# Kernel tuning notes

Hardware: AMD Instinct MI355X
Metric: run time of the kernel (lower is better)

## Reference

```python
import jax, jax.numpy as jnp
import numpy as np

VOCAB = 50257
D = 1024
EDGES = [0, 20000, 40000, VOCAB]  # cluster boundaries
HSZ = [1024, 256, 64]             # D // 4**i per cluster


def setup_inputs() -> dict:
    key = jax.random.key(0)
    ks = jax.random.split(key, 8)
    emb_input = jax.random.randint(ks[0], (8, 2048), 0, VOCAB, dtype=jnp.int64)
    inp = {"emb_input": emb_input}
    for i in range(3):
        vsz = EDGES[i + 1] - EDGES[i]
        h = HSZ[i]
        inp[f"emb{i}"] = jax.random.normal(ks[1 + 2 * i], (vsz, h), dtype=jnp.float32) * 0.02
        # nn.Linear(h, D, bias=False) weight has shape [D, h]
        inp[f"w{i}"] = jax.random.normal(ks[2 + 2 * i], (D, h), dtype=jnp.float32) * 0.02
    return inp


def reference(emb_input, emb0, w0, emb1, w1, emb2, w2):
    B, S = emb_input.shape
    idx = emb_input.reshape(-1)  # [N]
    clusters = [(emb0, w0), (emb1, w1), (emb2, w2)]
    out = jnp.zeros((idx.shape[0], D), dtype=jnp.float32)
    for i, (emb, w) in enumerate(clusters):
        lo, hi = EDGES[i], EDGES[i + 1]
        mask = (idx >= lo) & (idx < hi)                       # [N]
        local = jnp.clip(idx - lo, 0, emb.shape[0] - 1)       # in-range gather ids
        h = emb[local]                                        # [N, hsz_i]
        proj = jnp.einsum('nh,dh->nd', h, w)                  # [N, D]
        out = out + jnp.where(mask[:, None], proj, 0.0)
    return out.reshape(B, S, D)
```

## Files before the change

### kernel.cpp

```cpp
#include <hip/hip_runtime.h>
#include <stdint.h>

#define DOUT 1024
#define NMAX 16384

typedef __attribute__((ext_vector_type(8))) short short8;
typedef __attribute__((ext_vector_type(4))) float floatx4;

__device__ __forceinline__ unsigned short f2bf(float f) {
  union { float f; uint32_t u; } v;
  v.f = f;
  return (unsigned short)((v.u + 0x7FFFu + ((v.u >> 16) & 1u)) >> 16);
}

__global__ __launch_bounds__(256) void classify_cvt_kernel(
    const int* __restrict__ idx, int* __restrict__ cnt,
    int* __restrict__ bucket, int* __restrict__ blocal, int N,
    const float* __restrict__ w0, const float* __restrict__ w1,
    const float* __restrict__ w2, unsigned short* __restrict__ wb0,
    unsigned short* __restrict__ wb1, unsigned short* __restrict__ wb2) {
  if (blockIdx.x < 64) {
    int n = blockIdx.x * 256 + threadIdx.x;
    int lane = threadIdx.x & 63;
    int c = -1, v = 0;
    if (n < N) {
      v = idx[n];
      c = (v < 20000) ? 0 : ((v < 40000) ? 1 : 2);
    }
#pragma unroll
    for (int k = 0; k < 3; ++k) {
      unsigned long long m = __ballot(c == k);
      if (c == k) {
        int leader = __ffsll((unsigned long long)m) - 1;
        int base = 0;
        if (lane == leader) base = atomicAdd(&cnt[k], (int)__popcll(m));
        base = __shfl(base, leader);
        int rank = (int)__popcll(m & ((1ull << (unsigned)lane) - 1ull));
        int lo = (k == 0) ? 0 : (k == 1) ? 20000 : 40000;
        bucket[k * NMAX + base + rank] = n;
        blocal[k * NMAX + base + rank] = v - lo;
      }
    }
  } else {
    int i = (blockIdx.x - 64) * 256 + threadIdx.x;
    if (i >= 344064) return;
    const float4* src;
    ushort4* dst;
    if (i < 262144) {
      src = (const float4*)w0 + i;
      dst = (ushort4*)wb0 + i;
    } else if (i < 327680) {
      src = (const float4*)w1 + (i - 262144);
      dst = (ushort4*)wb1 + (i - 262144);
    } else {
      src = (const float4*)w2 + (i - 327680);
      dst = (ushort4*)wb2 + (i - 327680);
    }
    float4 v = *src;
    ushort4 o;
    o.x = f2bf(v.x); o.y = f2bf(v.y); o.z = f2bf(v.z); o.w = f2bf(v.w);
    *dst = o;
  }
}

__global__ __launch_bounds__(256) void gather_fused(
    const float* __restrict__ emb0, const float* __restrict__ emb1,
    const float* __restrict__ emb2, const int* __restrict__ blocal,
    const int* __restrict__ cnt, unsigned short* __restrict__ a0,
    unsigned short* __restrict__ a1, unsigned short* __restrict__ a2) {
  const int z = blockIdx.z;
  const int hshift = 10 - 2 * z;
  const float* emb = (z == 0) ? emb0 : (z == 1) ? emb1 : emb2;
  unsigned short* acomp = (z == 0) ? a0 : (z == 1) ? a1 : a2;
  const int* bl = blocal + z * NMAX;
  const int count = cnt[z];
  const int h4s = hshift - 2;
  const int total = count << h4s;
  for (int i = blockIdx.x * 256 + threadIdx.x; i < total; i += gridDim.x * 256) {
    int row = i >> h4s;
    int k4 = i & ((1 << h4s) - 1);
    int loc = bl[row];
    float4 v = ((const float4*)(emb + ((size_t)loc << hshift)))[k4];
    ushort4 o;
    o.x = f2bf(v.x); o.y = f2bf(v.y); o.z = f2bf(v.z); o.w = f2bf(v.w);
    ((ushort4*)(acomp + ((size_t)row << hshift)))[k4] = o;
  }
}

template <int H>
__device__ __forceinline__ void gemm_body(
    const unsigned short* __restrict__ A, const unsigned short* __restrict__ B,
    int count, const int* __restrict__ bucket, float* __restrict__ out,
    unsigned short* As, unsigned short* Bs, int* rowTok) {
  const int m0 = blockIdx.y * 64;
  if (m0 >= count) return;
  const int n0 = blockIdx.x * 128;

  const int tid = threadIdx.x;
  const int wave = tid >> 6;
  const int lane = tid & 63;
  const int quad = lane >> 4;
  const int l16 = lane & 15;
  const int wm = wave & 1;
  const int wn = wave >> 1;

  if (tid < 64) {
    int m = m0 + tid;
    rowTok[tid] = (m < count) ? bucket[m] : -1;
  }

  floatx4 acc[2][4];
#pragma unroll
  for (int i = 0; i < 2; ++i)
#pragma unroll
    for (int j = 0; j < 4; ++j) acc[i][j] = (floatx4){0.f, 0.f, 0.f, 0.f};

  const char* Ab = (const char*)A;
  const char* Bb = (const char*)B;
  const int row_lo = tid >> 2;
  const int ck = tid & 3;

  for (int k0 = 0; k0 < H; k0 += 64) {
    __syncthreads();
#pragma unroll
    for (int t = 0; t < 2; ++t) {
      const void* ga = Ab + ((size_t)(m0 + row_lo) * H + k0 + t * 32) * 2 + ck * 16;
      void* la = (char*)As + (t * 4096 + wave * 1024);
      __builtin_amdgcn_global_load_lds(
          (const __attribute__((address_space(1))) void*)ga,
          (__attribute__((address_space(3))) void*)la, 16, 0, 0);
    }
#pragma unroll
    for (int t = 0; t < 2; ++t)
#pragma unroll
      for (int p = 0; p < 2; ++p) {
        const void* gb =
            Bb + ((size_t)(n0 + p * 64 + row_lo) * H + k0 + t * 32) * 2 + ck * 16;
        void* lb = (char*)Bs + (t * 8192 + p * 4096 + wave * 1024);
        __builtin_amdgcn_global_load_lds(
            (const __attribute__((address_space(1))) void*)gb,
            (__attribute__((address_space(3))) void*)lb, 16, 0, 0);
      }
    __syncthreads();

#pragma unroll
    for (int t = 0; t < 2; ++t) {
      short8 af[2], bf[4];
#pragma unroll
      for (int mi = 0; mi < 2; ++mi)
        af[mi] = *(const short8*)&As[t * 2048 + (wm * 32 + mi * 16 + l16) * 32 + quad * 8];
#pragma unroll
      for (int ni = 0; ni < 4; ++ni)
        bf[ni] = *(const short8*)&Bs[t * 4096 + (wn * 64 + ni * 16 + l16) * 32 + quad * 8];
#pragma unroll
      for (int mi = 0; mi < 2; ++mi)
#pragma unroll
        for (int ni = 0; ni < 4; ++ni)
          acc[mi][ni] = __builtin_amdgcn_mfma_f32_16x16x32_bf16(
              af[mi], bf[ni], acc[mi][ni], 0, 0, 0);
    }
  }

  const int colBase = n0 + wn * 64 + l16;
#pragma unroll
  for (int mi = 0; mi < 2; ++mi) {
#pragma unroll
    for (int r = 0; r < 4; ++r) {
      int tok = rowTok[wm * 32 + mi * 16 + quad * 4 + r];
      if (tok >= 0) {
        float* o = out + (size_t)tok * DOUT + colBase;
#pragma unroll
        for (int ni = 0; ni < 4; ++ni) o[ni * 16] = acc[mi][ni][r];
      }
    }
  }
}

__global__ __launch_bounds__(256) void gemm_fused(
    const unsigned short* __restrict__ a0, const unsigned short* __restrict__ a1,
    const unsigned short* __restrict__ a2, const unsigned short* __restrict__ wb0,
    const unsigned short* __restrict__ wb1, const unsigned short* __restrict__ wb2,
    const int* __restrict__ cnt, const int* __restrict__ bucket,
    float* __restrict__ out) {
  __shared__ __align__(16) unsigned short As[2 * 64 * 32];
  __shared__ __align__(16) unsigned short Bs[2 * 128 * 32];
  __shared__ int rowTok[64];

  const int z = blockIdx.z;
  if (z == 0)
    gemm_body<1024>(a0, wb0, cnt[0], bucket + 0 * NMAX, out, As, Bs, rowTok);
  else if (z == 1)
    gemm_body<256>(a1, wb1, cnt[1], bucket + 1 * NMAX, out, As, Bs, rowTok);
  else
    gemm_body<64>(a2, wb2, cnt[2], bucket + 2 * NMAX, out, As, Bs, rowTok);
}

extern "C" void kernel_launch(void* const* d_in, const int* in_sizes, int n_in,
                              void* d_out, int out_size, void* d_ws, size_t ws_size,
                              hipStream_t stream) {
  const int* idx = (const int*)d_in[0];
  const float* emb0 = (const float*)d_in[1];
  const float* w0 = (const float*)d_in[2];
  const float* emb1 = (const float*)d_in[3];
  const float* w1 = (const float*)d_in[4];
  const float* emb2 = (const float*)d_in[5];
  const float* w2 = (const float*)d_in[6];
  float* out = (float*)d_out;
  const int N = in_sizes[0];

  char* ws = (char*)d_ws;
  int* cnt = (int*)ws;
  int* bucket = (int*)(ws + 1024);
  int* blocal = bucket + 3 * NMAX;
  size_t off = 1024 + (size_t)6 * NMAX * 4;
  off = (off + 255) & ~(size_t)255;
  unsigned short* wb0 = (unsigned short*)(ws + off); off += (size_t)DOUT * 1024 * 2;
  unsigned short* wb1 = (unsigned short*)(ws + off); off += (size_t)DOUT * 256 * 2;
  unsigned short* wb2 = (unsigned short*)(ws + off); off += (size_t)DOUT * 64 * 2;
  off = (off + 255) & ~(size_t)255;
  unsigned short* a0 = (unsigned short*)(ws + off); off += (size_t)NMAX * 1024 * 2;
  unsigned short* a1 = (unsigned short*)(ws + off); off += (size_t)NMAX * 256 * 2;
  unsigned short* a2 = (unsigned short*)(ws + off); off += (size_t)NMAX * 64 * 2;

  hipMemsetAsync(cnt, 0, 16 * sizeof(int), stream);

  classify_cvt_kernel<<<64 + 1344, 256, 0, stream>>>(
      idx, cnt, bucket, blocal, N, w0, w1, w2, wb0, wb1, wb2);

  dim3 ggrid(512, 1, 3);
  gather_fused<<<ggrid, 256, 0, stream>>>(emb0, emb1, emb2, blocal, cnt, a0, a1, a2);

  dim3 grid(DOUT / 128, NMAX / 64, 3);
  gemm_fused<<<grid, 256, 0, stream>>>(a0, a1, a2, wb0, wb1, wb2, cnt, bucket, out);
}
```

Before: 208.2 us.

## Fuse embedding gather and bf16 conversion into the GEMM A-tile load

```diff
diff --git a/kernel.cpp b/kernel.cpp
--- a/kernel.cpp
+++ b/kernel.cpp
@@ -1,4 +1,5 @@
 #include <hip/hip_runtime.h>
+#include <hip/hip_bf16.h>
 #include <stdint.h>
 
 #define DOUT 1024
@@ -11,6 +12,16 @@
   union { float f; uint32_t u; } v;
   v.f = f;
   return (unsigned short)((v.u + 0x7FFFu + ((v.u >> 16) & 1u)) >> 16);
+}
+
+__device__ __forceinline__ short8 cvt8(float4 a, float4 b) {
+  __hip_bfloat162 p0 = __float22bfloat162_rn(make_float2(a.x, a.y));
+  __hip_bfloat162 p1 = __float22bfloat162_rn(make_float2(a.z, a.w));
+  __hip_bfloat162 p2 = __float22bfloat162_rn(make_float2(b.x, b.y));
+  __hip_bfloat162 p3 = __float22bfloat162_rn(make_float2(b.z, b.w));
+  union { __hip_bfloat162 h[4]; short8 s; } u;
+  u.h[0] = p0; u.h[1] = p1; u.h[2] = p2; u.h[3] = p3;
+  return u.s;
 }
 
 __global__ __launch_bounds__(256) void classify_cvt_kernel(
@@ -63,35 +74,12 @@
   }
 }
 
-__global__ __launch_bounds__(256) void gather_fused(
-    const float* __restrict__ emb0, const float* __restrict__ emb1,
-    const float* __restrict__ emb2, const int* __restrict__ blocal,
-    const int* __restrict__ cnt, unsigned short* __restrict__ a0,
-    unsigned short* __restrict__ a1, unsigned short* __restrict__ a2) {
-  const int z = blockIdx.z;
-  const int hshift = 10 - 2 * z;
-  const float* emb = (z == 0) ? emb0 : (z == 1) ? emb1 : emb2;
-  unsigned short* acomp = (z == 0) ? a0 : (z == 1) ? a1 : a2;
-  const int* bl = blocal + z * NMAX;
-  const int count = cnt[z];
-  const int h4s = hshift - 2;
-  const int total = count << h4s;
-  for (int i = blockIdx.x * 256 + threadIdx.x; i < total; i += gridDim.x * 256) {
-    int row = i >> h4s;
-    int k4 = i & ((1 << h4s) - 1);
-    int loc = bl[row];
-    float4 v = ((const float4*)(emb + ((size_t)loc << hshift)))[k4];
-    ushort4 o;
-    o.x = f2bf(v.x); o.y = f2bf(v.y); o.z = f2bf(v.z); o.w = f2bf(v.w);
-    ((ushort4*)(acomp + ((size_t)row << hshift)))[k4] = o;
-  }
-}
-
 template <int H>
 __device__ __forceinline__ void gemm_body(
-    const unsigned short* __restrict__ A, const unsigned short* __restrict__ B,
-    int count, const int* __restrict__ bucket, float* __restrict__ out,
-    unsigned short* As, unsigned short* Bs, int* rowTok) {
+    const float* __restrict__ emb, const unsigned short* __restrict__ B,
+    int count, const int* __restrict__ bucket, const int* __restrict__ blocal,
+    float* __restrict__ out, unsigned short* As, unsigned short* Bs,
+    int* rowTok, int* rowLoc) {
   const int m0 = blockIdx.y * 64;
   if (m0 >= count) return;
   const int n0 = blockIdx.x * 128;
@@ -107,7 +95,9 @@
   if (tid < 64) {
     int m = m0 + tid;
     rowTok[tid] = (m < count) ? bucket[m] : -1;
-  }
+    rowLoc[tid] = (m < count) ? blocal[m] : 0;
+  }
+  __syncthreads();
 
   floatx4 acc[2][4];
 #pragma unroll
@@ -115,20 +105,20 @@
 #pragma unroll
     for (int j = 0; j < 4; ++j) acc[i][j] = (floatx4){0.f, 0.f, 0.f, 0.f};
 
-  const char* Ab = (const char*)A;
   const char* Bb = (const char*)B;
   const int row_lo = tid >> 2;
   const int ck = tid & 3;
 
+  const float* arow = emb + (size_t)rowLoc[row_lo] * H + ck * 8;
+
   for (int k0 = 0; k0 < H; k0 += 64) {
     __syncthreads();
 #pragma unroll
     for (int t = 0; t < 2; ++t) {
-      const void* ga = Ab + ((size_t)(m0 + row_lo) * H + k0 + t * 32) * 2 + ck * 16;
-      void* la = (char*)As + (t * 4096 + wave * 1024);
-      __builtin_amdgcn_global_load_lds(
-          (const __attribute__((address_space(1))) void*)ga,
-          (__attribute__((address_space(3))) void*)la, 16, 0, 0);
+      const float* src = arow + k0 + t * 32;
+      float4 v0 = *(const float4*)src;
+      float4 v1 = *(const float4*)(src + 4);
+      *(short8*)&As[t * 2048 + row_lo * 32 + ck * 8] = cvt8(v0, v1);
     }
 #pragma unroll
     for (int t = 0; t < 2; ++t)
@@ -177,22 +167,26 @@
 }
 
 __global__ __launch_bounds__(256) void gemm_fused(
-    const unsigned short* __restrict__ a0, const unsigned short* __restrict__ a1,
-    const unsigned short* __restrict__ a2, const unsigned short* __restrict__ wb0,
+    const float* __restrict__ emb0, const float* __restrict__ emb1,
+    const float* __restrict__ emb2, const unsigned short* __restrict__ wb0,
     const unsigned short* __restrict__ wb1, const unsigned short* __restrict__ wb2,
     const int* __restrict__ cnt, const int* __restrict__ bucket,
-    float* __restrict__ out) {
+    const int* __restrict__ blocal, float* __restrict__ out) {
   __shared__ __align__(16) unsigned short As[2 * 64 * 32];
   __shared__ __align__(16) unsigned short Bs[2 * 128 * 32];
   __shared__ int rowTok[64];
+  __shared__ int rowLoc[64];
 
   const int z = blockIdx.z;
   if (z == 0)
-    gemm_body<1024>(a0, wb0, cnt[0], bucket + 0 * NMAX, out, As, Bs, rowTok);
+    gemm_body<1024>(emb0, wb0, cnt[0], bucket + 0 * NMAX, blocal + 0 * NMAX,
+                    out, As, Bs, rowTok, rowLoc);
   else if (z == 1)
-    gemm_body<256>(a1, wb1, cnt[1], bucket + 1 * NMAX, out, As, Bs, rowTok);
+    gemm_body<256>(emb1, wb1, cnt[1], bucket + 1 * NMAX, blocal + 1 * NMAX,
+                   out, As, Bs, rowTok, rowLoc);
   else
-    gemm_body<64>(a2, wb2, cnt[2], bucket + 2 * NMAX, out, As, Bs, rowTok);
+    gemm_body<64>(emb2, wb2, cnt[2], bucket + 2 * NMAX, blocal + 2 * NMAX,
+                  out, As, Bs, rowTok, rowLoc);
 }
 
 extern "C" void kernel_launch(void* const* d_in, const int* in_sizes, int n_in,
@@ -217,19 +211,13 @@
   unsigned short* wb0 = (unsigned short*)(ws + off); off += (size_t)DOUT * 1024 * 2;
   unsigned short* wb1 = (unsigned short*)(ws + off); off += (size_t)DOUT * 256 * 2;
   unsigned short* wb2 = (unsigned short*)(ws + off); off += (size_t)DOUT * 64 * 2;
-  off = (off + 255) & ~(size_t)255;
-  unsigned short* a0 = (unsigned short*)(ws + off); off += (size_t)NMAX * 1024 * 2;
-  unsigned short* a1 = (unsigned short*)(ws + off); off += (size_t)NMAX * 256 * 2;
-  unsigned short* a2 = (unsigned short*)(ws + off); off += (size_t)NMAX * 64 * 2;
 
   hipMemsetAsync(cnt, 0, 16 * sizeof(int), stream);
 
   classify_cvt_kernel<<<64 + 1344, 256, 0, stream>>>(
       idx, cnt, bucket, blocal, N, w0, w1, w2, wb0, wb1, wb2);
 
-  dim3 ggrid(512, 1, 3);
-  gather_fused<<<ggrid, 256, 0, stream>>>(emb0, emb1, emb2, blocal, cnt, a0, a1, a2);
-
   dim3 grid(DOUT / 128, NMAX / 64, 3);
-  gemm_fused<<<grid, 256, 0, stream>>>(a0, a1, a2, wb0, wb1, wb2, cnt, bucket, out);
-}
+  gemm_fused<<<grid, 256, 0, stream>>>(emb0, emb1, emb2, wb0, wb1, wb2,
+                                       cnt, bucket, blocal, out);
+}
```

After: 205.6 us. About the same (-1.2%).
